# Performance work log

Hardware: AMD Instinct MI355X
Metric: run time of the kernel (lower is better)

Reference implementation:

```python
import jax, jax.numpy as jnp
import numpy as np

NEG_SLOPE = 0.01  # torch LeakyReLU default


def setup_inputs() -> dict:
    N, H, Da, A, E, T, M = 100000, 256, 128, 250000, 60000, 512, 20000
    key = jax.random.key(0)
    ks = jax.random.split(key, 10)
    inp = {
        "nodes_representations": jax.random.normal(ks[0], (N, H), dtype=jnp.float32),
        "hyperedge_arg_node_idxs": jax.random.randint(ks[1], (A,), 0, N),
        "unq_hyperedge_type_reprs": jax.random.normal(ks[2], (T, H), dtype=jnp.float32),
        "hyperedge_type_name_unq_idxs": jax.random.randint(ks[3], (E,), 0, T),
        "unq_hyperedge_arg_name_reprs": jax.random.normal(ks[4], (M, Da), dtype=jnp.float32),
        "hyperedge_arg_name_unq_idxs": jax.random.randint(ks[5], (A,), 0, M),
        "hyperedge_arg_to_edge_id": jax.random.randint(ks[6], (A,), 0, E),
        "num_edges": E,
        "W1": jax.random.normal(ks[7], (H + Da, H), dtype=jnp.float32) * 0.05,
        "b1": jnp.zeros((H,), dtype=jnp.float32),
        "W2": jax.random.normal(ks[8], (2 * H + Da, H), dtype=jnp.float32) * 0.05,
        "b2": jnp.zeros((H,), dtype=jnp.float32),
    }
    return inp


def reference(nodes_representations, hyperedge_arg_node_idxs, unq_hyperedge_type_reprs,
              hyperedge_type_name_unq_idxs, unq_hyperedge_arg_name_reprs,
              hyperedge_arg_name_unq_idxs, hyperedge_arg_to_edge_id, num_edges,
              W1, b1, W2, b2):
    # Gather per-arg name and node reprs, concat -> [A, Da+H]
    arg_name = unq_hyperedge_arg_name_reprs[hyperedge_arg_name_unq_idxs]
    arg_node = nodes_representations[hyperedge_arg_node_idxs]
    arg_reprs = jnp.concatenate([arg_name, arg_node], axis=-1)

    Da = arg_name.shape[1]
    # Edge type reprs [E, H], zero-padded to [E, H+Da] (branch always taken here)
    edge_type = unq_hyperedge_type_reprs[hyperedge_type_name_unq_idxs]
    edge_type = jnp.concatenate(
        [edge_type, jnp.zeros((edge_type.shape[0], Da), dtype=edge_type.dtype)], axis=-1)

    # Message MLP on stacked [A+E, H+Da]
    all_in = jnp.concatenate([arg_reprs, edge_type], axis=0)
    msgs = jax.nn.leaky_relu(all_in @ W1 + b1, negative_slope=NEG_SLOPE)

    # Segment-max grouped by edge id (every edge gets its own type message, so no empty segments)
    seg_ids = jnp.concatenate(
        [hyperedge_arg_to_edge_id, jnp.arange(num_edges, dtype=hyperedge_arg_to_edge_id.dtype)])
    edge_states = jax.ops.segment_max(msgs, seg_ids, num_segments=num_edges)

    # Update MLP: gather edge state per arg, concat with arg reprs -> [A, 2H+Da]
    # (Dropout is identity in eval mode.)
    upd_in = jnp.concatenate([edge_states[hyperedge_arg_to_edge_id], arg_reprs], axis=1)
    message_to_nodes = jax.nn.leaky_relu(upd_in @ W2 + b2, negative_slope=NEG_SLOPE)
    return (message_to_nodes, edge_states)
```

## Files before the change

### kernel.cpp

```cpp
#include <hip/hip_runtime.h>
#include <stdint.h>

#define A_CNT 250000
#define E_CNT 60000
#define N_NODES 100000
#define M_NAMES 20000
#define T_TYPES 512
#define H_DIM 256
#define DA    128
#define K1    384
#define K2    640
#define NEG_SLOPE 0.01f
#define SENT  0xFFFFFFFFu

typedef float v4f __attribute__((ext_vector_type(4)));
typedef short v8s __attribute__((ext_vector_type(8)));
typedef unsigned short u16;

__device__ __forceinline__ unsigned enc_f(float f) {
    unsigned u = __float_as_uint(f);
    return (u & 0x80000000u) ? ~u : (u | 0x80000000u);
}
__device__ __forceinline__ float dec_f(unsigned e) {
    unsigned u = (e & 0x80000000u) ? (e & 0x7FFFFFFFu) : ~e;
    return __uint_as_float(u);
}
__device__ __forceinline__ u16 f2bf(float f) {
    unsigned u = __float_as_uint(f);
    u += 0x7FFFu + ((u >> 16) & 1u);
    return (u16)(u >> 16);
}
__device__ __forceinline__ uint4 pack8(float4 a, float4 b) {
    union { u16 u[8]; uint4 v; } p;
    p.u[0]=f2bf(a.x); p.u[1]=f2bf(a.y); p.u[2]=f2bf(a.z); p.u[3]=f2bf(a.w);
    p.u[4]=f2bf(b.x); p.u[5]=f2bf(b.y); p.u[6]=f2bf(b.z); p.u[7]=f2bf(b.w);
    return p.v;
}

__device__ __forceinline__ void gload16(const u16* g, u16* l) {
    __builtin_amdgcn_global_load_lds(
        (const __attribute__((address_space(1))) unsigned int*)(g),
        (__attribute__((address_space(3))) unsigned int*)(l), 16, 0, 0);
}

__global__ void wprep_kernel(const float* __restrict__ W, u16* __restrict__ Wt, int K) {
    int k = blockIdx.x, c = threadIdx.x;
    Wt[(size_t)c * K + k] = f2bf(W[(size_t)k * 256 + c]);
}

__global__ void tobf16_kernel(const float* __restrict__ in, u16* __restrict__ out, int n8) {
    int i = blockIdx.x * 256 + threadIdx.x;
    if (i < n8) {
        const float4* p = (const float4*)in + (size_t)2 * i;
        float4 a = p[0], b = p[1];
        ((uint4*)out)[i] = pack8(a, b);
    }
}

__global__ void hist_kernel(const int* __restrict__ arg_edge, unsigned* __restrict__ counts) {
    int i = blockIdx.x * 256 + threadIdx.x;
    if (i < A_CNT) atomicAdd(&counts[arg_edge[i]], 1u);
}

__global__ __launch_bounds__(1024) void scan_kernel(const unsigned* __restrict__ counts,
                                                    unsigned* __restrict__ cursor) {
    __shared__ unsigned sd[1024];
    const int tid = threadIdx.x;
    const int CH = (E_CNT + 1023) / 1024;
    const int base = tid * CH;
    unsigned s = 0;
    for (int i = 0; i < CH; ++i) { int idx = base + i; if (idx < E_CNT) s += counts[idx]; }
    sd[tid] = s; __syncthreads();
    for (int d = 1; d < 1024; d <<= 1) {
        unsigned v = (tid >= d) ? sd[tid - d] : 0u; __syncthreads();
        sd[tid] += v; __syncthreads();
    }
    unsigned run = sd[tid] - s;
    for (int i = 0; i < CH; ++i) {
        int idx = base + i;
        if (idx < E_CNT) { cursor[idx] = run; run += counts[idx]; }
    }
}

__global__ void scatter_kernel(const int* __restrict__ arg_edge, unsigned* __restrict__ cursor,
                               unsigned* __restrict__ perm, unsigned* __restrict__ sorted_edge) {
    int i = blockIdx.x * 256 + threadIdx.x;
    if (i < A_CNT) {
        int e = arg_edge[i];
        unsigned pos = atomicAdd(&cursor[e], 1u);
        perm[pos] = (unsigned)i;
        sorted_edge[pos] = (unsigned)e;
    }
}

__global__ __launch_bounds__(256, 3) void gemm1_kernel(
    const u16* __restrict__ nodes_bf, const int* __restrict__ arg_node_idx,
    const u16* __restrict__ types_bf, const int* __restrict__ type_idx,
    const u16* __restrict__ names_bf, const int* __restrict__ arg_name_idx,
    const unsigned* __restrict__ perm, const unsigned* __restrict__ sorted_edge,
    const u16* __restrict__ Wt1, const float* __restrict__ b1,
    const u16* __restrict__ zbuf,
    unsigned* __restrict__ enc)
{
    __shared__ __align__(16) u16 sX[128 * 32];
    __shared__ __align__(16) u16 sW[128 * 32];
    const int t = threadIdx.x;
    const int lane = t & 63, wave = t >> 6;
    const int row0 = blockIdx.x * 128;
    const int col0 = blockIdx.y * 128;

    const int rsub = wave * 16 + (lane >> 2);
    const int slot = lane & 3;

    const u16* xs0[2]; const u16* xs1[2]; int xcls[2];
    const u16* ws[2];
    u16* xdst[2]; u16* wdst[2];
    #pragma unroll
    for (int c = 0; c < 2; ++c) {
        const int rloc = c * 64 + rsub;
        const int ss = slot ^ ((rloc >> 1) & 3);
        const int gr = row0 + rloc;
        if (gr < A_CNT) {
            int aid = (int)perm[gr];
            xcls[c] = 0;
            xs0[c] = names_bf + (size_t)arg_name_idx[aid] * DA + ss * 8;
            xs1[c] = nodes_bf + (size_t)arg_node_idx[aid] * H_DIM + ss * 8 - DA;
        } else if (gr < A_CNT + E_CNT) {
            xcls[c] = 1;
            xs0[c] = types_bf + (size_t)type_idx[gr - A_CNT] * H_DIM + ss * 8;
            xs1[c] = zbuf;
        } else {
            xcls[c] = 2; xs0[c] = zbuf; xs1[c] = zbuf;
        }
        ws[c]   = Wt1 + (size_t)(col0 + rloc) * K1 + ss * 8;
        xdst[c] = &sX[(c * 64 + wave * 16) * 32];
        wdst[c] = &sW[(c * 64 + wave * 16) * 32];
    }

    const int wr = (wave & 1) * 64, wc = (wave >> 1) * 64;
    const int lm = lane & 15, lq = lane >> 4;

    int xoff[4], woff[4];
    #pragma unroll
    for (int i = 0; i < 4; ++i) {
        int ra = wr + i * 16 + lm;
        xoff[i] = ra * 32 + (lq ^ ((ra >> 1) & 3)) * 8;
        int rb = wc + i * 16 + lm;
        woff[i] = rb * 32 + (lq ^ ((rb >> 1) & 3)) * 8;
    }

    v4f acc[4][4];
    #pragma unroll
    for (int i = 0; i < 4; ++i)
        #pragma unroll
        for (int j = 0; j < 4; ++j) acc[i][j] = (v4f)0.f;

    for (int kc = 0; kc < K1; kc += 32) {
        #pragma unroll
        for (int c = 0; c < 2; ++c) {
            const u16* xsrc;
            if (xcls[c] == 0)      xsrc = ((kc < DA) ? xs0[c] : xs1[c]) + kc;
            else if (xcls[c] == 1) xsrc = (kc < H_DIM) ? (xs0[c] + kc) : zbuf;
            else                   xsrc = zbuf;
            gload16(xsrc, xdst[c]);
            gload16(ws[c] + kc, wdst[c]);
        }
        __syncthreads();

        v8s af[4], bf[4];
        #pragma unroll
        for (int i = 0; i < 4; ++i) af[i] = *(const v8s*)&sX[xoff[i]];
        #pragma unroll
        for (int j = 0; j < 4; ++j) bf[j] = *(const v8s*)&sW[woff[j]];
        #pragma unroll
        for (int i = 0; i < 4; ++i)
            #pragma unroll
            for (int j = 0; j < 4; ++j)
                acc[i][j] = __builtin_amdgcn_mfma_f32_16x16x32_bf16(af[i], bf[j], acc[i][j], 0, 0, 0);
        __syncthreads();
    }

    float bb[4];
    #pragma unroll
    for (int j = 0; j < 4; ++j) bb[j] = b1[col0 + wc + j*16 + lm];

    #pragma unroll
    for (int i = 0; i < 4; ++i) {
        const int r0 = row0 + wr + i*16 + lq*4;
        unsigned seg[4];
        #pragma unroll
        for (int reg = 0; reg < 4; ++reg) {
            int g = r0 + reg;
            seg[reg] = (g < A_CNT) ? sorted_edge[g]
                     : (g < A_CNT + E_CNT ? (unsigned)(g - A_CNT) : SENT);
        }
        #pragma unroll
        for (int j = 0; j < 4; ++j) {
            const int cj = col0 + wc + j*16 + lm;
            float v[4];
            #pragma unroll
            for (int reg = 0; reg < 4; ++reg) {
                float y = acc[i][j][reg] + bb[j];
                v[reg] = (y >= 0.f) ? y : NEG_SLOPE * y;
            }
            unsigned cs = seg[0]; float m = v[0];
            #pragma unroll
            for (int reg = 1; reg < 4; ++reg) {
                if (seg[reg] == cs) { m = fmaxf(m, v[reg]); }
                else {
                    if (cs != SENT) atomicMax(&enc[(size_t)cs * H_DIM + cj], enc_f(m));
                    cs = seg[reg]; m = v[reg];
                }
            }
            if (cs != SENT) atomicMax(&enc[(size_t)cs * H_DIM + cj], enc_f(m));
        }
    }
}

__global__ void decode_kernel(unsigned* __restrict__ enc, u16* __restrict__ es_bf) {
    size_t i = (size_t)blockIdx.x * 1024 + threadIdx.x;
    const size_t n4 = (size_t)E_CNT * H_DIM / 4;
    if (i < n4) {
        uint4 e = ((const uint4*)enc)[i];
        float4 f;
        f.x = dec_f(e.x); f.y = dec_f(e.y); f.z = dec_f(e.z); f.w = dec_f(e.w);
        ((float4*)enc)[i] = f;
        union { u16 u[4]; unsigned long long v; } p;
        p.u[0]=f2bf(f.x); p.u[1]=f2bf(f.y); p.u[2]=f2bf(f.z); p.u[3]=f2bf(f.w);
        ((unsigned long long*)es_bf)[i] = p.v;
    }
}

__global__ __launch_bounds__(256, 3) void gemm2_kernel(
    const u16* __restrict__ nodes_bf, const int* __restrict__ arg_node_idx,
    const u16* __restrict__ names_bf, const int* __restrict__ arg_name_idx,
    const int* __restrict__ arg_edge, const u16* __restrict__ es_bf,
    const u16* __restrict__ Wt2, const float* __restrict__ b2,
    const u16* __restrict__ zbuf,
    float* __restrict__ out)
{
    __shared__ __align__(16) u16 sX[128 * 32];
    __shared__ __align__(16) u16 sW[128 * 32];
    const int t = threadIdx.x;
    const int lane = t & 63, wave = t >> 6;
    const int row0 = blockIdx.x * 128;
    const int col0 = blockIdx.y * 128;

    const int rsub = wave * 16 + (lane >> 2);
    const int slot = lane & 3;

    const u16* pe[2]; const u16* pn[2]; const u16* pd[2]; int valid[2];
    const u16* ws[2];
    u16* xdst[2]; u16* wdst[2];
    #pragma unroll
    for (int c = 0; c < 2; ++c) {
        const int rloc = c * 64 + rsub;
        const int ss = slot ^ ((rloc >> 1) & 3);
        const int gr = row0 + rloc;
        if (gr < A_CNT) {
            valid[c] = 1;
            pe[c] = es_bf   + (size_t)arg_edge[gr]      * H_DIM + ss * 8;
            pn[c] = names_bf + (size_t)arg_name_idx[gr] * DA    + ss * 8 - H_DIM;
            pd[c] = nodes_bf + (size_t)arg_node_idx[gr] * H_DIM + ss * 8 - H_DIM - DA;
        } else {
            valid[c] = 0; pe[c] = zbuf; pn[c] = zbuf; pd[c] = zbuf;
        }
        ws[c]   = Wt2 + (size_t)(col0 + rloc) * K2 + ss * 8;
        xdst[c] = &sX[(c * 64 + wave * 16) * 32];
        wdst[c] = &sW[(c * 64 + wave * 16) * 32];
    }

    const int wr = (wave & 1) * 64, wc = (wave >> 1) * 64;
    const int lm = lane & 15, lq = lane >> 4;

    int xoff[4], woff[4];
    #pragma unroll
    for (int i = 0; i < 4; ++i) {
        int ra = wr + i * 16 + lm;
        xoff[i] = ra * 32 + (lq ^ ((ra >> 1) & 3)) * 8;
        int rb = wc + i * 16 + lm;
        woff[i] = rb * 32 + (lq ^ ((rb >> 1) & 3)) * 8;
    }

    v4f acc[4][4];
    #pragma unroll
    for (int i = 0; i < 4; ++i)
        #pragma unroll
        for (int j = 0; j < 4; ++j) acc[i][j] = (v4f)0.f;

    for (int kc = 0; kc < K2; kc += 32) {
        #pragma unroll
        for (int c = 0; c < 2; ++c) {
            const u16* xsrc;
            if (valid[c]) {
                const u16* p = (kc < H_DIM) ? pe[c] : ((kc < H_DIM + DA) ? pn[c] : pd[c]);
                xsrc = p + kc;
            } else xsrc = zbuf;
            gload16(xsrc, xdst[c]);
            gload16(ws[c] + kc, wdst[c]);
        }
        __syncthreads();

        v8s af[4], bf[4];
        #pragma unroll
        for (int i = 0; i < 4; ++i) af[i] = *(const v8s*)&sX[xoff[i]];
        #pragma unroll
        for (int j = 0; j < 4; ++j) bf[j] = *(const v8s*)&sW[woff[j]];
        #pragma unroll
        for (int i = 0; i < 4; ++i)
            #pragma unroll
            for (int j = 0; j < 4; ++j)
                acc[i][j] = __builtin_amdgcn_mfma_f32_16x16x32_bf16(af[i], bf[j], acc[i][j], 0, 0, 0);
        __syncthreads();
    }

    float bb[4];
    #pragma unroll
    for (int j = 0; j < 4; ++j) bb[j] = b2[col0 + wc + j*16 + lm];

    #pragma unroll
    for (int i = 0; i < 4; ++i) {
        const int r0 = row0 + wr + i*16 + lq*4;
        #pragma unroll
        for (int reg = 0; reg < 4; ++reg) {
            const int g = r0 + reg;
            if (g < A_CNT) {
                #pragma unroll
                for (int j = 0; j < 4; ++j) {
                    float y = acc[i][j][reg] + bb[j];
                    y = (y >= 0.f) ? y : NEG_SLOPE * y;
                    out[(size_t)g * H_DIM + col0 + wc + j*16 + lm] = y;
                }
            }
        }
    }
}

extern "C" void kernel_launch(void* const* d_in, const int* in_sizes, int n_in,
                              void* d_out, int out_size, void* d_ws, size_t ws_size,
                              hipStream_t stream) {
    const float* nodes        = (const float*)d_in[0];
    const int*   arg_node_idx = (const int*)  d_in[1];
    const float* types        = (const float*)d_in[2];
    const int*   type_idx     = (const int*)  d_in[3];
    const float* names        = (const float*)d_in[4];
    const int*   arg_name_idx = (const int*)  d_in[5];
    const int*   arg_edge     = (const int*)  d_in[6];
    const float* W1           = (const float*)d_in[8];
    const float* b1           = (const float*)d_in[9];
    const float* W2           = (const float*)d_in[10];
    const float* b2           = (const float*)d_in[11];

    float* out_msg = (float*)d_out;
    float* out_es  = out_msg + (size_t)A_CNT * H_DIM;
    unsigned* enc  = (unsigned*)out_es;

    char* ws = (char*)d_ws;
    size_t off = 0;
    auto alloc = [&](size_t bytes) -> void* {
        void* p = ws + off;
        off = (off + bytes + 255) & ~(size_t)255;
        return p;
    };
    u16* Wt1          = (u16*)alloc((size_t)256 * K1 * sizeof(u16));
    u16* Wt2          = (u16*)alloc((size_t)256 * K2 * sizeof(u16));
    u16* es_bf        = (u16*)alloc((size_t)E_CNT * H_DIM * sizeof(u16));
    u16* nodes_bf     = (u16*)alloc((size_t)N_NODES * H_DIM * sizeof(u16));
    u16* names_bf     = (u16*)alloc((size_t)M_NAMES * DA * sizeof(u16));
    u16* types_bf     = (u16*)alloc((size_t)T_TYPES * H_DIM * sizeof(u16));
    u16* zbuf         = (u16*)alloc(256);
    unsigned* counts  = (unsigned*)alloc((size_t)E_CNT * sizeof(unsigned));
    unsigned* cursor  = (unsigned*)alloc((size_t)E_CNT * sizeof(unsigned));
    unsigned* perm    = (unsigned*)alloc((size_t)A_CNT * sizeof(unsigned));
    unsigned* sorted_edge = (unsigned*)alloc((size_t)A_CNT * sizeof(unsigned));

    hipMemsetAsync(counts, 0, (size_t)E_CNT * sizeof(unsigned), stream);
    hipMemsetAsync(enc, 0, (size_t)E_CNT * H_DIM * sizeof(unsigned), stream);
    hipMemsetAsync(zbuf, 0, 256, stream);

    wprep_kernel<<<K1, 256, 0, stream>>>(W1, Wt1, K1);
    wprep_kernel<<<K2, 256, 0, stream>>>(W2, Wt2, K2);
    {
        int n8 = N_NODES * H_DIM / 8;
        tobf16_kernel<<<(n8 + 255) / 256, 256, 0, stream>>>(nodes, nodes_bf, n8);
    }
    {
        int n8 = M_NAMES * DA / 8;
        tobf16_kernel<<<(n8 + 255) / 256, 256, 0, stream>>>(names, names_bf, n8);
    }
    {
        int n8 = T_TYPES * H_DIM / 8;
        tobf16_kernel<<<(n8 + 255) / 256, 256, 0, stream>>>(types, types_bf, n8);
    }
    hist_kernel<<<(A_CNT + 255) / 256, 256, 0, stream>>>(arg_edge, counts);
    scan_kernel<<<1, 1024, 0, stream>>>(counts, cursor);
    scatter_kernel<<<(A_CNT + 255) / 256, 256, 0, stream>>>(arg_edge, cursor, perm, sorted_edge);

    dim3 g1((A_CNT + E_CNT + 127) / 128, 2);
    gemm1_kernel<<<g1, 256, 0, stream>>>(nodes_bf, arg_node_idx, types_bf, type_idx,
                                         names_bf, arg_name_idx, perm, sorted_edge,
                                         Wt1, b1, zbuf, enc);
    decode_kernel<<<((E_CNT * H_DIM / 4) + 1023) / 1024, 1024, 0, stream>>>(enc, es_bf);

    dim3 g2((A_CNT + 127) / 128, 2);
    gemm2_kernel<<<g2, 256, 0, stream>>>(nodes_bf, arg_node_idx, names_bf, arg_name_idx,
                                         arg_edge, es_bf, Wt2, b2, zbuf, out_msg);
}
```

Measured before the change: 877.2 us.

## Double-buffer LDS tiles in both GEMM kernels to overlap loads with MFMA

```diff
diff --git a/kernel.cpp b/kernel.cpp
--- a/kernel.cpp
+++ b/kernel.cpp
@@ -12,6 +12,7 @@
 #define K2    640
 #define NEG_SLOPE 0.01f
 #define SENT  0xFFFFFFFFu
+#define LDSZ  (128 * 32)
 
 typedef float v4f __attribute__((ext_vector_type(4)));
 typedef short v8s __attribute__((ext_vector_type(8)));
@@ -93,7 +94,7 @@
     }
 }
 
-__global__ __launch_bounds__(256, 3) void gemm1_kernel(
+__global__ __launch_bounds__(256, 5) void gemm1_kernel(
     const u16* __restrict__ nodes_bf, const int* __restrict__ arg_node_idx,
     const u16* __restrict__ types_bf, const int* __restrict__ type_idx,
     const u16* __restrict__ names_bf, const int* __restrict__ arg_name_idx,
@@ -102,8 +103,8 @@
     const u16* __restrict__ zbuf,
     unsigned* __restrict__ enc)
 {
-    __shared__ __align__(16) u16 sX[128 * 32];
-    __shared__ __align__(16) u16 sW[128 * 32];
+    __shared__ __align__(16) u16 sX[2 * LDSZ];
+    __shared__ __align__(16) u16 sW[2 * LDSZ];
     const int t = threadIdx.x;
     const int lane = t & 63, wave = t >> 6;
     const int row0 = blockIdx.x * 128;
@@ -155,29 +156,46 @@
         #pragma unroll
         for (int j = 0; j < 4; ++j) acc[i][j] = (v4f)0.f;
 
-    for (int kc = 0; kc < K1; kc += 32) {
+    auto stage = [&](int buf, int kc) {
         #pragma unroll
         for (int c = 0; c < 2; ++c) {
             const u16* xsrc;
             if (xcls[c] == 0)      xsrc = ((kc < DA) ? xs0[c] : xs1[c]) + kc;
             else if (xcls[c] == 1) xsrc = (kc < H_DIM) ? (xs0[c] + kc) : zbuf;
             else                   xsrc = zbuf;
-            gload16(xsrc, xdst[c]);
-            gload16(ws[c] + kc, wdst[c]);
-        }
-        __syncthreads();
-
+            gload16(xsrc, xdst[c] + buf * LDSZ);
+            gload16(ws[c] + kc, wdst[c] + buf * LDSZ);
+        }
+    };
+
+    const int nt = K1 / 32;
+    stage(0, 0);
+    for (int tt = 0; tt < nt; ++tt) {
+        if (tt + 1 < nt) {
+            stage((tt + 1) & 1, (tt + 1) * 32);
+            asm volatile("s_waitcnt vmcnt(4)" ::: "memory");
+        } else {
+            asm volatile("s_waitcnt vmcnt(0)" ::: "memory");
+        }
+        __builtin_amdgcn_sched_barrier(0);
+        __builtin_amdgcn_s_barrier();
+        __builtin_amdgcn_sched_barrier(0);
+
+        const u16* bx = &sX[(tt & 1) * LDSZ];
+        const u16* bw = &sW[(tt & 1) * LDSZ];
         v8s af[4], bf[4];
         #pragma unroll
-        for (int i = 0; i < 4; ++i) af[i] = *(const v8s*)&sX[xoff[i]];
-        #pragma unroll
-        for (int j = 0; j < 4; ++j) bf[j] = *(const v8s*)&sW[woff[j]];
+        for (int i = 0; i < 4; ++i) af[i] = *(const v8s*)&bx[xoff[i]];
+        #pragma unroll
+        for (int j = 0; j < 4; ++j) bf[j] = *(const v8s*)&bw[woff[j]];
         #pragma unroll
         for (int i = 0; i < 4; ++i)
             #pragma unroll
             for (int j = 0; j < 4; ++j)
                 acc[i][j] = __builtin_amdgcn_mfma_f32_16x16x32_bf16(af[i], bf[j], acc[i][j], 0, 0, 0);
-        __syncthreads();
+
+        __builtin_amdgcn_sched_barrier(0);
+        __builtin_amdgcn_s_barrier();
     }
 
     float bb[4];
@@ -231,7 +249,7 @@
     }
 }
 
-__global__ __launch_bounds__(256, 3) void gemm2_kernel(
+__global__ __launch_bounds__(256, 5) void gemm2_kernel(
     const u16* __restrict__ nodes_bf, const int* __restrict__ arg_node_idx,
     const u16* __restrict__ names_bf, const int* __restrict__ arg_name_idx,
     const int* __restrict__ arg_edge, const u16* __restrict__ es_bf,
@@ -239,8 +257,8 @@
     const u16* __restrict__ zbuf,
     float* __restrict__ out)
 {
-    __shared__ __align__(16) u16 sX[128 * 32];
-    __shared__ __align__(16) u16 sW[128 * 32];
+    __shared__ __align__(16) u16 sX[2 * LDSZ];
+    __shared__ __align__(16) u16 sW[2 * LDSZ];
     const int t = threadIdx.x;
     const int lane = t & 63, wave = t >> 6;
     const int row0 = blockIdx.x * 128;
@@ -288,7 +306,7 @@
         #pragma unroll
         for (int j = 0; j < 4; ++j) acc[i][j] = (v4f)0.f;
 
-    for (int kc = 0; kc < K2; kc += 32) {
+    auto stage = [&](int buf, int kc) {
         #pragma unroll
         for (int c = 0; c < 2; ++c) {
             const u16* xsrc;
@@ -296,22 +314,39 @@
                 const u16* p = (kc < H_DIM) ? pe[c] : ((kc < H_DIM + DA) ? pn[c] : pd[c]);
                 xsrc = p + kc;
             } else xsrc = zbuf;
-            gload16(xsrc, xdst[c]);
-            gload16(ws[c] + kc, wdst[c]);
-        }
-        __syncthreads();
-
+            gload16(xsrc, xdst[c] + buf * LDSZ);
+            gload16(ws[c] + kc, wdst[c] + buf * LDSZ);
+        }
+    };
+
+    const int nt = K2 / 32;
+    stage(0, 0);
+    for (int tt = 0; tt < nt; ++tt) {
+        if (tt + 1 < nt) {
+            stage((tt + 1) & 1, (tt + 1) * 32);
+            asm volatile("s_waitcnt vmcnt(4)" ::: "memory");
+        } else {
+            asm volatile("s_waitcnt vmcnt(0)" ::: "memory");
+        }
+        __builtin_amdgcn_sched_barrier(0);
+        __builtin_amdgcn_s_barrier();
+        __builtin_amdgcn_sched_barrier(0);
+
+        const u16* bx = &sX[(tt & 1) * LDSZ];
+        const u16* bw = &sW[(tt & 1) * LDSZ];
         v8s af[4], bf[4];
         #pragma unroll
-        for (int i = 0; i < 4; ++i) af[i] = *(const v8s*)&sX[xoff[i]];
-        #pragma unroll
-        for (int j = 0; j < 4; ++j) bf[j] = *(const v8s*)&sW[woff[j]];
+        for (int i = 0; i < 4; ++i) af[i] = *(const v8s*)&bx[xoff[i]];
+        #pragma unroll
+        for (int j = 0; j < 4; ++j) bf[j] = *(const v8s*)&bw[woff[j]];
         #pragma unroll
         for (int i = 0; i < 4; ++i)
             #pragma unroll
             for (int j = 0; j < 4; ++j)
                 acc[i][j] = __builtin_amdgcn_mfma_f32_16x16x32_bf16(af[i], bf[j], acc[i][j], 0, 0, 0);
-        __syncthreads();
+
+        __builtin_amdgcn_sched_barrier(0);
+        __builtin_amdgcn_s_barrier();
     }
 
     float bb[4];
```

New measurement: 1.013 ms. 1.15x slower.
